# Performance work log

Hardware: AMD Instinct MI355X
Metric: run time of the kernel (lower is better)

The kernel has to match this reference:

```python
import jax, jax.numpy as jnp
import numpy as np

E = 8        # n_routed_experts
TOPK = 2     # num_experts_per_tok


def setup_inputs() -> dict:
    key = jax.random.key(0)
    k0, k1, k2, k3, k4 = jax.random.split(key, 5)
    B, S, D, H = 1, 2048, 1024, 2816
    scale = 0.02
    x = jax.random.normal(k0, (B, S, D), jnp.float32)
    Wg = jax.random.normal(k1, (E, D), jnp.float32) * scale   # gate weight [E, D]
    W1 = jax.random.normal(k2, (E, H, D), jnp.float32) * scale  # up-gate proj
    W2 = jax.random.normal(k3, (E, D, H), jnp.float32) * scale  # down proj
    W3 = jax.random.normal(k4, (E, H, D), jnp.float32) * scale  # up proj
    return {"x": x, "Wg": Wg, "W1": W1, "W2": W2, "W3": W3}


def _moe_forward(x, Wg, W1, W2, W3):
    B, S, D = x.shape
    xt = x.reshape(-1, D)                      # [T, D], T = B*S
    T = xt.shape[0]
    # --- gate: logits -> softmax -> top-k, normalized top-k weights ---
    logits = xt @ Wg.T                         # [T, E]
    scores = jax.nn.softmax(logits, axis=-1)
    w, idx = jax.lax.top_k(scores, TOPK)       # [T, K]
    w = w / (w.sum(axis=-1, keepdims=True) + 1e-20)
    # combine weights per token per expert (scatter top-k weights) [T, E]
    cw = jnp.zeros((T, E), xt.dtype).at[jnp.arange(T)[:, None], idx].add(w)
    # --- per-expert SwiGLU FFN (batched over experts) ---
    h = jax.nn.silu(jnp.einsum('td,ehd->teh', xt, W1)) * jnp.einsum('td,ehd->teh', xt, W3)  # [T,E,H]
    out = jnp.einsum('teh,edh->ted', h, W2)    # [T, E, D]
    # weighted combine of selected experts (cw is zero for unselected)
    y = jnp.einsum('te,ted->td', cw, out)      # [T, D]
    return y.reshape(B, S, D)


def reference(x, Wg, W1, W2, W3):
    return _moe_forward(x, Wg, W1, W2, W3)
```

## Files before the change

### kernel.cpp

```cpp
#include <hip/hip_runtime.h>
#include <hip/hip_bf16.h>

#define T_TOK 2048
#define D_DIM 1024
#define H_DIM 2816
#define E_NUM 8
#define CAP   1024

typedef __attribute__((ext_vector_type(8))) short short8;
typedef __attribute__((ext_vector_type(4))) float floatx4;

__device__ __forceinline__ unsigned short f2bf(float f) {
    unsigned int b = __float_as_uint(f);
    b += 0x7FFFu + ((b >> 16) & 1u);
    return (unsigned short)(b >> 16);
}

__device__ __forceinline__ short8 pack8(float4 a, float4 b) {
    short8 o;
    o[0] = (short)f2bf(a.x); o[1] = (short)f2bf(a.y);
    o[2] = (short)f2bf(a.z); o[3] = (short)f2bf(a.w);
    o[4] = (short)f2bf(b.x); o[5] = (short)f2bf(b.y);
    o[6] = (short)f2bf(b.z); o[7] = (short)f2bf(b.w);
    return o;
}

__device__ __forceinline__ void gl2lds16(const void* g, void* l) {
    __builtin_amdgcn_global_load_lds(
        (const __attribute__((address_space(1))) unsigned int*)g,
        (__attribute__((address_space(3))) unsigned int*)l,
        16, 0, 0);
}


__global__ __launch_bounds__(256) void k_gate2(const float* __restrict__ x,
                                               const float* __restrict__ Wg,
                                               float* __restrict__ topw,
                                               int* __restrict__ tpos,
                                               int* __restrict__ counts,
                                               unsigned short* __restrict__ xg) {
    const int wave = threadIdx.x >> 6, lane = threadIdx.x & 63;
    const int t = blockIdx.x * 4 + wave;
    const float* xr = x + (size_t)t * D_DIM;
    float acc[E_NUM];
#pragma unroll
    for (int e = 0; e < E_NUM; ++e) acc[e] = 0.f;
#pragma unroll 4
    for (int i = 0; i < D_DIM / 64; ++i) {
        float xv = xr[lane + 64 * i];
#pragma unroll
        for (int e = 0; e < E_NUM; ++e) acc[e] += xv * Wg[e * D_DIM + lane + 64 * i];
    }
#pragma unroll
    for (int e = 0; e < E_NUM; ++e) {
#pragma unroll
        for (int s = 32; s > 0; s >>= 1) acc[e] += __shfl_xor(acc[e], s, 64);
    }
    int slot0 = 0, slot1 = 0;
    if (lane == 0) {
        float mx = acc[0];
#pragma unroll
        for (int e = 1; e < E_NUM; ++e) mx = fmaxf(mx, acc[e]);
        float p[E_NUM], s = 0.f;
#pragma unroll
        for (int e = 0; e < E_NUM; ++e) { p[e] = __expf(acc[e] - mx); s += p[e]; }
        int i0 = 0;
#pragma unroll
        for (int e = 1; e < E_NUM; ++e) if (p[e] > p[i0]) i0 = e;
        int i1 = (i0 == 0) ? 1 : 0;
#pragma unroll
        for (int e = 0; e < E_NUM; ++e) if (e != i0 && p[e] > p[i1]) i1 = e;
        float s0 = p[i0] / s, s1 = p[i1] / s;
        float d = s0 + s1 + 1e-20f;
        int p0 = atomicAdd(&counts[i0], 1); if (p0 >= CAP) p0 = CAP - 1;
        int p1 = atomicAdd(&counts[i1], 1); if (p1 >= CAP) p1 = CAP - 1;
        slot0 = i0 * CAP + p0;
        slot1 = i1 * CAP + p1;
        tpos[t * 2] = slot0; tpos[t * 2 + 1] = slot1;
        topw[t * 2] = s0 / d; topw[t * 2 + 1] = s1 / d;
    }
    slot0 = __shfl(slot0, 0, 64);
    slot1 = __shfl(slot1, 0, 64);
    const float4* xr4 = (const float4*)xr;
    ushort4* xg4 = (ushort4*)xg;
#pragma unroll
    for (int it = 0; it < 4; ++it) {
        float4 v = xr4[lane + 64 * it];
        ushort4 o;
        o.x = f2bf(v.x); o.y = f2bf(v.y); o.z = f2bf(v.z); o.w = f2bf(v.w);
        xg4[(size_t)slot0 * 256 + lane + 64 * it] = o;
        xg4[(size_t)slot1 * 256 + lane + 64 * it] = o;
    }
}

__global__ __launch_bounds__(256, 2) void k_gemm13(const unsigned short* __restrict__ xg,
                                                   const float* __restrict__ W1,
                                                   const float* __restrict__ W3,
                                                   const int* __restrict__ counts,
                                                   unsigned short* __restrict__ U) {
    const int nt = blockIdx.x;
    const int mt = blockIdx.y;
    const int e  = blockIdx.z;
    const int cnt = min(counts[e], CAP);
    if (mt * 256 >= cnt) return;

    __shared__ __align__(16) unsigned char As[32 * 1056];
    __shared__ __align__(16) unsigned char Bs[16 * 1056];

    const int tid = threadIdx.x, lane = tid & 63, wave = tid >> 6;
    const int fr = lane & 15, quad = lane >> 4, f7 = fr & 7, f8 = fr >> 3;

    const unsigned short* aBase = xg
        + ((size_t)e * CAP + mt * 256 + wave * 64 + (lane >> 3)) * D_DIM
        + ((lane & 7) ^ (lane >> 3)) * 8;

    const int brow = tid >> 1, bhalf = tid & 1;
    const float* wrow = (brow < 64)
        ? W1 + ((size_t)e * H_DIM + nt * 64 + brow) * D_DIM
        : W3 + ((size_t)e * H_DIM + nt * 64 + brow - 64) * D_DIM;
    const int bg0 = (brow >> 3) * 1056 + (brow & 7) * 128;
    const int br7 = brow & 7;

    floatx4 acc[4][8];
#pragma unroll
    for (int m = 0; m < 4; ++m)
#pragma unroll
        for (int n = 0; n < 8; ++n) acc[m][n] = (floatx4)0.f;

#pragma unroll 1
    for (int k0 = 0; k0 < D_DIM; k0 += 64) {
#pragma unroll
        for (int j = 0; j < 8; ++j)
            gl2lds16(aBase + (size_t)j * 8 * D_DIM + k0, As + (wave * 8 + j) * 1056);
#pragma unroll
        for (int j = 0; j < 4; ++j) {
            int c = bhalf * 4 + j;
            float4 lo = *(const float4*)(wrow + k0 + c * 8);
            float4 hi = *(const float4*)(wrow + k0 + c * 8 + 4);
            *(short8*)(Bs + bg0 + ((c ^ br7) << 4)) = pack8(lo, hi);
        }
        __syncthreads();
#pragma unroll
        for (int kk = 0; kk < 2; ++kk) {
            const int cA = (((kk * 4) | quad) ^ f7) << 4;
            short8 a[4];
#pragma unroll
            for (int m = 0; m < 4; ++m)
                a[m] = *(const short8*)(As + (wave * 8 + m * 2 + f8) * 1056 + f7 * 128 + cA);
            short8 b[8];
#pragma unroll
            for (int n = 0; n < 8; ++n)
                b[n] = *(const short8*)(Bs + (n * 2 + f8) * 1056 + f7 * 128 + cA);
#pragma unroll
            for (int m = 0; m < 4; ++m)
#pragma unroll
                for (int n = 0; n < 8; ++n)
                    acc[m][n] = __builtin_amdgcn_mfma_f32_16x16x32_bf16(a[m], b[n], acc[m][n], 0, 0, 0);
        }
        __syncthreads();
    }

#pragma unroll
    for (int m = 0; m < 4; ++m) {
#pragma unroll
        for (int r = 0; r < 4; ++r) {
            int g = mt * 256 + wave * 64 + m * 16 + quad * 4 + r;
            if (g < cnt) {
                size_t rowb = ((size_t)e * CAP + g) * H_DIM + nt * 64;
#pragma unroll
                for (int f = 0; f < 4; ++f) {
                    float u1 = acc[m][f][r], u3 = acc[m][f + 4][r];
                    float u = u1 / (1.f + __expf(-u1)) * u3;
                    U[rowb + f * 16 + fr] = f2bf(u);
                }
            }
        }
    }
}

__global__ __launch_bounds__(256) void k_gemm2(const unsigned short* __restrict__ U,
                                               const float* __restrict__ W2,
                                               const int* __restrict__ counts,
                                               float* __restrict__ Yp) {
    const int nt = blockIdx.x;
    const int mt = blockIdx.y;
    const int e  = blockIdx.z;
    const int cnt = min(counts[e], CAP);
    if (mt * 128 >= cnt) return;

    __shared__ __align__(16) unsigned char As[16 * 1056];
    __shared__ __align__(16) unsigned char Bs[16 * 1056];

    const int tid = threadIdx.x, lane = tid & 63, wave = tid >> 6;
    const int fr = lane & 15, quad = lane >> 4, f7 = fr & 7, f8 = fr >> 3;
    const int wr = wave & 1, wc = wave >> 1;

    const unsigned short* aBase = U
        + ((size_t)e * CAP + mt * 128 + wave * 32 + (lane >> 3)) * H_DIM
        + ((lane & 7) ^ (lane >> 3)) * 8;

    const int brow = tid >> 1, bhalf = tid & 1;
    const float* wrow = W2 + ((size_t)e * D_DIM + nt * 128 + brow) * H_DIM;
    const int bg0 = (brow >> 3) * 1056 + (brow & 7) * 128;
    const int br7 = brow & 7;

    floatx4 acc[4][4];
#pragma unroll
    for (int m = 0; m < 4; ++m)
#pragma unroll
        for (int n = 0; n < 4; ++n) acc[m][n] = (floatx4)0.f;

#pragma unroll 1
    for (int k0 = 0; k0 < H_DIM; k0 += 64) {
#pragma unroll
        for (int j = 0; j < 4; ++j)
            gl2lds16(aBase + (size_t)j * 8 * H_DIM + k0, As + (wave * 4 + j) * 1056);
#pragma unroll
        for (int j = 0; j < 4; ++j) {
            int c = bhalf * 4 + j;
            float4 lo = *(const float4*)(wrow + k0 + c * 8);
            float4 hi = *(const float4*)(wrow + k0 + c * 8 + 4);
            *(short8*)(Bs + bg0 + ((c ^ br7) << 4)) = pack8(lo, hi);
        }
        __syncthreads();
#pragma unroll
        for (int kk = 0; kk < 2; ++kk) {
            const int cA = (((kk * 4) | quad) ^ f7) << 4;
            short8 a[4];
#pragma unroll
            for (int m = 0; m < 4; ++m)
                a[m] = *(const short8*)(As + (wr * 8 + m * 2 + f8) * 1056 + f7 * 128 + cA);
            short8 b[4];
#pragma unroll
            for (int n = 0; n < 4; ++n)
                b[n] = *(const short8*)(Bs + (wc * 8 + n * 2 + f8) * 1056 + f7 * 128 + cA);
#pragma unroll
            for (int m = 0; m < 4; ++m)
#pragma unroll
                for (int n = 0; n < 4; ++n)
                    acc[m][n] = __builtin_amdgcn_mfma_f32_16x16x32_bf16(a[m], b[n], acc[m][n], 0, 0, 0);
        }
        __syncthreads();
    }

#pragma unroll
    for (int m = 0; m < 4; ++m) {
#pragma unroll
        for (int r = 0; r < 4; ++r) {
            int g = mt * 128 + wr * 64 + m * 16 + quad * 4 + r;
            if (g < cnt) {
                size_t rowb = ((size_t)e * CAP + g) * D_DIM + nt * 128 + wc * 64;
#pragma unroll
                for (int n = 0; n < 4; ++n)
                    Yp[rowb + n * 16 + fr] = acc[m][n][r];
            }
        }
    }
}

__global__ __launch_bounds__(256) void k_combine(const float* __restrict__ Yp,
                                                 const int* __restrict__ tpos,
                                                 const float* __restrict__ topw,
                                                 float* __restrict__ y) {
    int i = blockIdx.x * 256 + threadIdx.x;
    int t = i >> 8, c = i & 255;
    int p0 = tpos[t * 2], p1 = tpos[t * 2 + 1];
    float w0 = topw[t * 2], w1 = topw[t * 2 + 1];
    float4 a = ((const float4*)Yp)[(size_t)p0 * 256 + c];
    float4 b = ((const float4*)Yp)[(size_t)p1 * 256 + c];
    float4 o;
    o.x = w0 * a.x + w1 * b.x;
    o.y = w0 * a.y + w1 * b.y;
    o.z = w0 * a.z + w1 * b.z;
    o.w = w0 * a.w + w1 * b.w;
    ((float4*)y)[i] = o;
}

static const size_t OFF_XG   = 0;
static const size_t OFF_U    = (size_t)E_NUM * CAP * D_DIM * 2;
static const size_t OFF_YP   = OFF_U + (size_t)E_NUM * CAP * H_DIM * 2;
static const size_t OFF_TOPW = OFF_YP + (size_t)E_NUM * CAP * D_DIM * 4;
static const size_t OFF_TPOS = OFF_TOPW + 16384;
static const size_t OFF_META = OFF_TPOS + 16384;

extern "C" void kernel_launch(void* const* d_in, const int* in_sizes, int n_in,
                              void* d_out, int out_size, void* d_ws, size_t ws_size,
                              hipStream_t stream) {
    const float* x  = (const float*)d_in[0];
    const float* Wg = (const float*)d_in[1];
    const float* W1 = (const float*)d_in[2];
    const float* W2 = (const float*)d_in[3];
    const float* W3 = (const float*)d_in[4];
    float* y = (float*)d_out;
    char* ws = (char*)d_ws;

    unsigned short* xg = (unsigned short*)(ws + OFF_XG);
    unsigned short* U  = (unsigned short*)(ws + OFF_U);
    float* Yp   = (float*)(ws + OFF_YP);
    float* topw = (float*)(ws + OFF_TOPW);
    int*   tpos = (int*)(ws + OFF_TPOS);
    int*   counts = (int*)(ws + OFF_META);

    hipMemsetAsync(counts, 0, 64, stream);

    k_gate2<<<T_TOK / 4, 256, 0, stream>>>(x, Wg, topw, tpos, counts, xg);
    k_gemm13<<<dim3(H_DIM / 64, CAP / 256, E_NUM), 256, 0, stream>>>(xg, W1, W3, counts, U);
    k_gemm2<<<dim3(D_DIM / 128, CAP / 128, E_NUM), 256, 0, stream>>>(U, W2, counts, Yp);
    k_combine<<<T_TOK * D_DIM / (256 * 4), 256, 0, stream>>>(Yp, tpos, topw, y);
}
```

Measured before the change: 500.3 us.

## Fuse weighted combine into down-proj via atomics, shrink tiles, prefetch weights

The separate combine kernel and the Yp buffer are gone. The down-projection epilogue now looks up each slot's token and gate weight and atomically adds its weighted output into a zeroed y. Both GEMMs use smaller M/N tiles to launch more blocks, and they prefetch the next fp32 weight slice into registers before the barrier to overlap global loads with compute. This removes a full write and read of the per-slot output, at the cost of an extra memset of y and fp32 atomic contention. Results also become nondeterministic in summation order.

```diff
diff --git a/kernel.cpp b/kernel.cpp
--- a/kernel.cpp
+++ b/kernel.cpp
@@ -35,8 +35,8 @@
 
 __global__ __launch_bounds__(256) void k_gate2(const float* __restrict__ x,
                                                const float* __restrict__ Wg,
-                                               float* __restrict__ topw,
-                                               int* __restrict__ tpos,
+                                               int* __restrict__ stok,
+                                               float* __restrict__ sw,
                                                int* __restrict__ counts,
                                                unsigned short* __restrict__ xg) {
     const int wave = threadIdx.x >> 6, lane = threadIdx.x & 63;
@@ -76,8 +76,8 @@
         int p1 = atomicAdd(&counts[i1], 1); if (p1 >= CAP) p1 = CAP - 1;
         slot0 = i0 * CAP + p0;
         slot1 = i1 * CAP + p1;
-        tpos[t * 2] = slot0; tpos[t * 2 + 1] = slot1;
-        topw[t * 2] = s0 / d; topw[t * 2 + 1] = s1 / d;
+        stok[slot0] = t; sw[slot0] = s0 / d;
+        stok[slot1] = t; sw[slot1] = s1 / d;
     }
     slot0 = __shfl(slot0, 0, 64);
     slot1 = __shfl(slot1, 0, 64);
@@ -93,25 +93,25 @@
     }
 }
 
-__global__ __launch_bounds__(256, 2) void k_gemm13(const unsigned short* __restrict__ xg,
-                                                   const float* __restrict__ W1,
-                                                   const float* __restrict__ W3,
-                                                   const int* __restrict__ counts,
-                                                   unsigned short* __restrict__ U) {
+__global__ __launch_bounds__(256) void k_gemm13(const unsigned short* __restrict__ xg,
+                                                const float* __restrict__ W1,
+                                                const float* __restrict__ W3,
+                                                const int* __restrict__ counts,
+                                                unsigned short* __restrict__ U) {
     const int nt = blockIdx.x;
     const int mt = blockIdx.y;
     const int e  = blockIdx.z;
     const int cnt = min(counts[e], CAP);
-    if (mt * 256 >= cnt) return;
-
-    __shared__ __align__(16) unsigned char As[32 * 1056];
+    if (mt * 128 >= cnt) return;
+
+    __shared__ __align__(16) unsigned char As[16 * 1056];
     __shared__ __align__(16) unsigned char Bs[16 * 1056];
 
     const int tid = threadIdx.x, lane = tid & 63, wave = tid >> 6;
     const int fr = lane & 15, quad = lane >> 4, f7 = fr & 7, f8 = fr >> 3;
 
     const unsigned short* aBase = xg
-        + ((size_t)e * CAP + mt * 256 + wave * 64 + (lane >> 3)) * D_DIM
+        + ((size_t)e * CAP + mt * 128 + wave * 32 + (lane >> 3)) * D_DIM
         + ((lane & 7) ^ (lane >> 3)) * 8;
 
     const int brow = tid >> 1, bhalf = tid & 1;
@@ -121,38 +121,52 @@
     const int bg0 = (brow >> 3) * 1056 + (brow & 7) * 128;
     const int br7 = brow & 7;
 
-    floatx4 acc[4][8];
-#pragma unroll
-    for (int m = 0; m < 4; ++m)
+    float4 breg[8];
+#pragma unroll
+    for (int j = 0; j < 4; ++j) {
+        int c = bhalf * 4 + j;
+        breg[2 * j]     = *(const float4*)(wrow + c * 8);
+        breg[2 * j + 1] = *(const float4*)(wrow + c * 8 + 4);
+    }
+
+    floatx4 acc[2][8];
+#pragma unroll
+    for (int m = 0; m < 2; ++m)
 #pragma unroll
         for (int n = 0; n < 8; ++n) acc[m][n] = (floatx4)0.f;
 
 #pragma unroll 1
     for (int k0 = 0; k0 < D_DIM; k0 += 64) {
 #pragma unroll
-        for (int j = 0; j < 8; ++j)
-            gl2lds16(aBase + (size_t)j * 8 * D_DIM + k0, As + (wave * 8 + j) * 1056);
+        for (int j = 0; j < 4; ++j)
+            gl2lds16(aBase + (size_t)j * 8 * D_DIM + k0, As + (wave * 4 + j) * 1056);
 #pragma unroll
         for (int j = 0; j < 4; ++j) {
             int c = bhalf * 4 + j;
-            float4 lo = *(const float4*)(wrow + k0 + c * 8);
-            float4 hi = *(const float4*)(wrow + k0 + c * 8 + 4);
-            *(short8*)(Bs + bg0 + ((c ^ br7) << 4)) = pack8(lo, hi);
+            *(short8*)(Bs + bg0 + ((c ^ br7) << 4)) = pack8(breg[2 * j], breg[2 * j + 1]);
+        }
+        if (k0 + 64 < D_DIM) {
+#pragma unroll
+            for (int j = 0; j < 4; ++j) {
+                int c = bhalf * 4 + j;
+                breg[2 * j]     = *(const float4*)(wrow + k0 + 64 + c * 8);
+                breg[2 * j + 1] = *(const float4*)(wrow + k0 + 64 + c * 8 + 4);
+            }
         }
         __syncthreads();
 #pragma unroll
         for (int kk = 0; kk < 2; ++kk) {
             const int cA = (((kk * 4) | quad) ^ f7) << 4;
-            short8 a[4];
-#pragma unroll
-            for (int m = 0; m < 4; ++m)
-                a[m] = *(const short8*)(As + (wave * 8 + m * 2 + f8) * 1056 + f7 * 128 + cA);
+            short8 a[2];
+#pragma unroll
+            for (int m = 0; m < 2; ++m)
+                a[m] = *(const short8*)(As + (wave * 4 + m * 2 + f8) * 1056 + f7 * 128 + cA);
             short8 b[8];
 #pragma unroll
             for (int n = 0; n < 8; ++n)
                 b[n] = *(const short8*)(Bs + (n * 2 + f8) * 1056 + f7 * 128 + cA);
 #pragma unroll
-            for (int m = 0; m < 4; ++m)
+            for (int m = 0; m < 2; ++m)
 #pragma unroll
                 for (int n = 0; n < 8; ++n)
                     acc[m][n] = __builtin_amdgcn_mfma_f32_16x16x32_bf16(a[m], b[n], acc[m][n], 0, 0, 0);
@@ -161,10 +175,10 @@
     }
 
 #pragma unroll
-    for (int m = 0; m < 4; ++m) {
+    for (int m = 0; m < 2; ++m) {
 #pragma unroll
         for (int r = 0; r < 4; ++r) {
-            int g = mt * 256 + wave * 64 + m * 16 + quad * 4 + r;
+            int g = mt * 128 + wave * 32 + m * 16 + quad * 4 + r;
             if (g < cnt) {
                 size_t rowb = ((size_t)e * CAP + g) * H_DIM + nt * 64;
 #pragma unroll
@@ -181,7 +195,9 @@
 __global__ __launch_bounds__(256) void k_gemm2(const unsigned short* __restrict__ U,
                                                const float* __restrict__ W2,
                                                const int* __restrict__ counts,
-                                               float* __restrict__ Yp) {
+                                               const int* __restrict__ stok,
+                                               const float* __restrict__ sw,
+                                               float* __restrict__ y) {
     const int nt = blockIdx.x;
     const int mt = blockIdx.y;
     const int e  = blockIdx.z;
@@ -189,24 +205,31 @@
     if (mt * 128 >= cnt) return;
 
     __shared__ __align__(16) unsigned char As[16 * 1056];
-    __shared__ __align__(16) unsigned char Bs[16 * 1056];
+    __shared__ __align__(16) unsigned char Bs[8 * 1056];
 
     const int tid = threadIdx.x, lane = tid & 63, wave = tid >> 6;
     const int fr = lane & 15, quad = lane >> 4, f7 = fr & 7, f8 = fr >> 3;
-    const int wr = wave & 1, wc = wave >> 1;
 
     const unsigned short* aBase = U
         + ((size_t)e * CAP + mt * 128 + wave * 32 + (lane >> 3)) * H_DIM
         + ((lane & 7) ^ (lane >> 3)) * 8;
 
-    const int brow = tid >> 1, bhalf = tid & 1;
-    const float* wrow = W2 + ((size_t)e * D_DIM + nt * 128 + brow) * H_DIM;
+    const int brow = tid >> 2, bq = tid & 3;
+    const float* wrow = W2 + ((size_t)e * D_DIM + nt * 64 + brow) * H_DIM;
     const int bg0 = (brow >> 3) * 1056 + (brow & 7) * 128;
     const int br7 = brow & 7;
 
-    floatx4 acc[4][4];
-#pragma unroll
-    for (int m = 0; m < 4; ++m)
+    float4 breg[4];
+#pragma unroll
+    for (int j = 0; j < 2; ++j) {
+        int c = bq * 2 + j;
+        breg[2 * j]     = *(const float4*)(wrow + c * 8);
+        breg[2 * j + 1] = *(const float4*)(wrow + c * 8 + 4);
+    }
+
+    floatx4 acc[2][4];
+#pragma unroll
+    for (int m = 0; m < 2; ++m)
 #pragma unroll
         for (int n = 0; n < 4; ++n) acc[m][n] = (floatx4)0.f;
 
@@ -216,26 +239,32 @@
         for (int j = 0; j < 4; ++j)
             gl2lds16(aBase + (size_t)j * 8 * H_DIM + k0, As + (wave * 4 + j) * 1056);
 #pragma unroll
-        for (int j = 0; j < 4; ++j) {
-            int c = bhalf * 4 + j;
-            float4 lo = *(const float4*)(wrow + k0 + c * 8);
-            float4 hi = *(const float4*)(wrow + k0 + c * 8 + 4);
-            *(short8*)(Bs + bg0 + ((c ^ br7) << 4)) = pack8(lo, hi);
+        for (int j = 0; j < 2; ++j) {
+            int c = bq * 2 + j;
+            *(short8*)(Bs + bg0 + ((c ^ br7) << 4)) = pack8(breg[2 * j], breg[2 * j + 1]);
+        }
+        if (k0 + 64 < H_DIM) {
+#pragma unroll
+            for (int j = 0; j < 2; ++j) {
+                int c = bq * 2 + j;
+                breg[2 * j]     = *(const float4*)(wrow + k0 + 64 + c * 8);
+                breg[2 * j + 1] = *(const float4*)(wrow + k0 + 64 + c * 8 + 4);
+            }
         }
         __syncthreads();
 #pragma unroll
         for (int kk = 0; kk < 2; ++kk) {
             const int cA = (((kk * 4) | quad) ^ f7) << 4;
-            short8 a[4];
-#pragma unroll
-            for (int m = 0; m < 4; ++m)
-                a[m] = *(const short8*)(As + (wr * 8 + m * 2 + f8) * 1056 + f7 * 128 + cA);
+            short8 a[2];
+#pragma unroll
+            for (int m = 0; m < 2; ++m)
+                a[m] = *(const short8*)(As + (wave * 4 + m * 2 + f8) * 1056 + f7 * 128 + cA);
             short8 b[4];
 #pragma unroll
             for (int n = 0; n < 4; ++n)
-                b[n] = *(const short8*)(Bs + (wc * 8 + n * 2 + f8) * 1056 + f7 * 128 + cA);
-#pragma unroll
-            for (int m = 0; m < 4; ++m)
+                b[n] = *(const short8*)(Bs + (n * 2 + f8) * 1056 + f7 * 128 + cA);
+#pragma unroll
+            for (int m = 0; m < 2; ++m)
 #pragma unroll
                 for (int n = 0; n < 4; ++n)
                     acc[m][n] = __builtin_amdgcn_mfma_f32_16x16x32_bf16(a[m], b[n], acc[m][n], 0, 0, 0);
@@ -244,44 +273,28 @@
     }
 
 #pragma unroll
-    for (int m = 0; m < 4; ++m) {
+    for (int m = 0; m < 2; ++m) {
 #pragma unroll
         for (int r = 0; r < 4; ++r) {
-            int g = mt * 128 + wr * 64 + m * 16 + quad * 4 + r;
+            int g = mt * 128 + wave * 32 + m * 16 + quad * 4 + r;
             if (g < cnt) {
-                size_t rowb = ((size_t)e * CAP + g) * D_DIM + nt * 128 + wc * 64;
+                int slot = e * CAP + g;
+                int t = stok[slot];
+                float w = sw[slot];
+                float* yr = y + (size_t)t * D_DIM + nt * 64;
 #pragma unroll
                 for (int n = 0; n < 4; ++n)
-                    Yp[rowb + n * 16 + fr] = acc[m][n][r];
+                    atomicAdd(&yr[n * 16 + fr], w * acc[m][n][r]);
             }
         }
     }
-}
-
-__global__ __launch_bounds__(256) void k_combine(const float* __restrict__ Yp,
-                                                 const int* __restrict__ tpos,
-                                                 const float* __restrict__ topw,
-                                                 float* __restrict__ y) {
-    int i = blockIdx.x * 256 + threadIdx.x;
-    int t = i >> 8, c = i & 255;
-    int p0 = tpos[t * 2], p1 = tpos[t * 2 + 1];
-    float w0 = topw[t * 2], w1 = topw[t * 2 + 1];
-    float4 a = ((const float4*)Yp)[(size_t)p0 * 256 + c];
-    float4 b = ((const float4*)Yp)[(size_t)p1 * 256 + c];
-    float4 o;
-    o.x = w0 * a.x + w1 * b.x;
-    o.y = w0 * a.y + w1 * b.y;
-    o.z = w0 * a.z + w1 * b.z;
-    o.w = w0 * a.w + w1 * b.w;
-    ((float4*)y)[i] = o;
 }
 
 static const size_t OFF_XG   = 0;
 static const size_t OFF_U    = (size_t)E_NUM * CAP * D_DIM * 2;
-static const size_t OFF_YP   = OFF_U + (size_t)E_NUM * CAP * H_DIM * 2;
-static const size_t OFF_TOPW = OFF_YP + (size_t)E_NUM * CAP * D_DIM * 4;
-static const size_t OFF_TPOS = OFF_TOPW + 16384;
-static const size_t OFF_META = OFF_TPOS + 16384;
+static const size_t OFF_STOK = OFF_U + (size_t)E_NUM * CAP * H_DIM * 2;
+static const size_t OFF_SW   = OFF_STOK + (size_t)E_NUM * CAP * 4;
+static const size_t OFF_META = OFF_SW + (size_t)E_NUM * CAP * 4;
 
 extern "C" void kernel_launch(void* const* d_in, const int* in_sizes, int n_in,
                               void* d_out, int out_size, void* d_ws, size_t ws_size,
@@ -296,15 +309,14 @@
 
     unsigned short* xg = (unsigned short*)(ws + OFF_XG);
     unsigned short* U  = (unsigned short*)(ws + OFF_U);
-    float* Yp   = (float*)(ws + OFF_YP);
-    float* topw = (float*)(ws + OFF_TOPW);
-    int*   tpos = (int*)(ws + OFF_TPOS);
+    int*   stok   = (int*)(ws + OFF_STOK);
+    float* sw     = (float*)(ws + OFF_SW);
     int*   counts = (int*)(ws + OFF_META);
 
     hipMemsetAsync(counts, 0, 64, stream);
-
-    k_gate2<<<T_TOK / 4, 256, 0, stream>>>(x, Wg, topw, tpos, counts, xg);
-    k_gemm13<<<dim3(H_DIM / 64, CAP / 256, E_NUM), 256, 0, stream>>>(xg, W1, W3, counts, U);
-    k_gemm2<<<dim3(D_DIM / 128, CAP / 128, E_NUM), 256, 0, stream>>>(U, W2, counts, Yp);
-    k_combine<<<T_TOK * D_DIM / (256 * 4), 256, 0, stream>>>(Yp, tpos, topw, y);
-}
+    hipMemsetAsync(y, 0, (size_t)T_TOK * D_DIM * sizeof(float), stream);
+
+    k_gate2<<<T_TOK / 4, 256, 0, stream>>>(x, Wg, stok, sw, counts, xg);
+    k_gemm13<<<dim3(H_DIM / 64, CAP / 128, E_NUM), 256, 0, stream>>>(xg, W1, W3, counts, U);
+    k_gemm2<<<dim3(D_DIM / 64, CAP / 128, E_NUM), 256, 0, stream>>>(U, W2, counts, stok, sw, y);
+}
```

New measurement: 543.0 us. +8.5%, slower.
